# Kernel optimization log

Measured on AMD Instinct MI355X. Metric: run time of the kernel, lower is better.

## Reference

```python
import jax, jax.numpy as jnp
import numpy as np

N = 100000      # nodes
E = 1600000     # edges (before self loops)
F_IN = 128
HID = 32
H = 4
OUT = 32
NEG_SLOPE = 0.2


def setup_inputs() -> dict:
    key = jax.random.key(0)
    ks = jax.random.split(key, 10)
    x = jax.random.normal(ks[0], (N, F_IN), jnp.float32)
    edge_index = jax.random.randint(ks[1], (2, E), 0, N, jnp.int32)
    s1 = 1.0 / np.sqrt(F_IN)
    s2 = 1.0 / np.sqrt(H * HID)
    W1 = jax.random.normal(ks[2], (F_IN, H * HID), jnp.float32) * s1
    a_src1 = jax.random.normal(ks[3], (H, HID), jnp.float32) * 0.1
    a_dst1 = jax.random.normal(ks[4], (H, HID), jnp.float32) * 0.1
    b1 = jnp.zeros((H * HID,), jnp.float32)
    W2 = jax.random.normal(ks[5], (H * HID, OUT), jnp.float32) * s2
    a_src2 = jax.random.normal(ks[6], (1, OUT), jnp.float32) * 0.1
    a_dst2 = jax.random.normal(ks[7], (1, OUT), jnp.float32) * 0.1
    b2 = jnp.zeros((OUT,), jnp.float32)
    return {"x": x, "edge_index": edge_index, "W1": W1, "a_src1": a_src1,
            "a_dst1": a_dst1, "b1": b1, "W2": W2, "a_src2": a_src2,
            "a_dst2": a_dst2, "b2": b2}


def gat_conv(x, src, dst, W, a_src, a_dst, b, heads, out_ch):
    # PyG GATConv (concat=True) with self loops already appended to src/dst.
    n = x.shape[0]
    h = (x @ W).reshape(n, heads, out_ch)                 # [N,H,C]
    alpha_s = jnp.sum(h * a_src, axis=-1)                 # [N,H]
    alpha_d = jnp.sum(h * a_dst, axis=-1)                 # [N,H]
    e = jax.nn.leaky_relu(alpha_s[src] + alpha_d[dst], NEG_SLOPE)  # [E',H]
    # segment softmax over destination nodes (self loops => every segment nonempty)
    emax = jax.ops.segment_max(e, dst, num_segments=n)
    ex = jnp.exp(e - emax[dst])
    denom = jax.ops.segment_sum(ex, dst, num_segments=n)
    alpha = ex / denom[dst]                               # [E',H]
    msg = h[src] * alpha[:, :, None]                      # [E',H,C]
    out = jax.ops.segment_sum(msg, dst, num_segments=n)   # [N,H,C]
    return out.reshape(n, heads * out_ch) + b


def reference(x, edge_index, W1, a_src1, a_dst1, b1, W2, a_src2, a_dst2, b2):
    loops = jnp.arange(N, dtype=edge_index.dtype)
    src = jnp.concatenate([edge_index[0], loops])
    dst = jnp.concatenate([edge_index[1], loops])
    h = gat_conv(x, src, dst, W1, a_src1, a_dst1, b1, H, HID)
    h = jax.nn.relu(h)                                    # dropout: eval mode, no-op
    out = gat_conv(h, src, dst, W2, a_src2, a_dst2, b2, 1, OUT)
    return out
```

## Files before the change

### kernel.cpp

```cpp
#include <hip/hip_runtime.h>
#include <hip/hip_fp16.h>

#define NEG 0.2f
#define EPB 4096
#define BSH 6
#define SLOT 48
#define CAP 1280
#define KBMAX 1664

typedef _Float16 half8 __attribute__((ext_vector_type(8)));
typedef float f32x4 __attribute__((ext_vector_type(4)));

__device__ inline __half2 pun_h2(float f) { union { float f; __half2 h; } u; u.f = f; return u.h; }
__device__ inline float pun_f(__half2 h) { union { float f; __half2 h; } u; u.h = h; return u.f; }

__global__ void k_prep(const float* __restrict__ W1, const float* __restrict__ W2,
                       half8* __restrict__ Wp, half8* __restrict__ W2p,
                       int* __restrict__ gcount, int KB) {
    int b = blockIdx.x;
    if (b < 8) {
        int u = b * 256 + threadIdx.x;
        int s = u >> 9, tn = (u >> 6) & 7, lane = u & 63;
        int quad = lane >> 4, c = lane & 15;
        half8 v;
#pragma unroll
        for (int j = 0; j < 8; ++j)
            v[j] = (_Float16)W1[(s * 32 + quad * 8 + j) * 128 + tn * 16 + c];
        Wp[u] = v;
    } else if (b < 10) {
        int u = (b - 8) * 256 + threadIdx.x;
        int n = u >> 8, s = (u >> 6) & 3, lane = u & 63;
        int quad = lane >> 4, c = lane & 15;
        half8 v;
#pragma unroll
        for (int j = 0; j < 8; ++j)
            v[j] = (_Float16)W2[(s * 32 + quad * 8 + j) * 32 + n * 16 + c];
        W2p[u] = v;
    } else {
        int i = (b - 10) * 256 + threadIdx.x;
        if (i < KB) gcount[i] = 0;
    }
}

__global__ __launch_bounds__(256) void k_pA(const float* __restrict__ x,
                                            const half8* __restrict__ Wp,
                                            const float* __restrict__ a_s,
                                            const float* __restrict__ a_d,
                                            __half* __restrict__ h1h,
                                            float* __restrict__ as1,
                                            float* __restrict__ ad1, int N,
                                            const int* __restrict__ srcp,
                                            const int* __restrict__ dstp,
                                            int* __restrict__ gcount,
                                            int2* __restrict__ ebuf,
                                            int E, int KB, int ngemm) {
    __shared__ _Float16 xa[64][136];
    __shared__ int lh[KBMAX];
    int t = threadIdx.x;

    if (blockIdx.x >= ngemm) {
        int blk = blockIdx.x - ngemm;
        int base0 = blk * EPB;
        int ss[16], dd[16];
#pragma unroll
        for (int j = 0; j < 16; ++j) {
            int i = base0 + j * 256 + t;
            if (i < E) { ss[j] = srcp[i]; dd[j] = dstp[i]; } else dd[j] = -1;
        }
        for (int i = t; i < KB; i += 256) lh[i] = 0;
        __syncthreads();
#pragma unroll
        for (int j = 0; j < 16; ++j)
            if (dd[j] >= 0) atomicAdd(&lh[dd[j] >> BSH], 1);
        __syncthreads();
        for (int b = t; b < KB; b += 256) {
            int c = lh[b];
            if (c > 0) lh[b] = atomicAdd(&gcount[b], c);
        }
        __syncthreads();
#pragma unroll
        for (int j = 0; j < 16; ++j) {
            if (dd[j] >= 0) {
                int b = dd[j] >> BSH;
                int pos = atomicAdd(&lh[b], 1);
                ebuf[(size_t)b * CAP + pos] = int2{ss[j], dd[j]};
            }
        }
        return;
    }

    int row0 = blockIdx.x * 64;
    {
        int row = t >> 2;
        int col0 = (t & 3) * 32;
        int gr = row0 + row;
        const float4* xsrc = (const float4*)&x[(size_t)gr * 128 + col0];
#pragma unroll
        for (int m = 0; m < 4; ++m) {
            float4 p0, p1;
            if (gr < N) { p0 = xsrc[m * 2]; p1 = xsrc[m * 2 + 1]; }
            else { p0 = float4{0,0,0,0}; p1 = float4{0,0,0,0}; }
            _Float16* dstq = &xa[row][col0 + m * 8];
            dstq[0] = (_Float16)p0.x; dstq[1] = (_Float16)p0.y;
            dstq[2] = (_Float16)p0.z; dstq[3] = (_Float16)p0.w;
            dstq[4] = (_Float16)p1.x; dstq[5] = (_Float16)p1.y;
            dstq[6] = (_Float16)p1.z; dstq[7] = (_Float16)p1.w;
        }
    }
    __syncthreads();

    int w = t >> 6;
    int lane = t & 63;
    int quad = lane >> 4, c = lane & 15;

    f32x4 acc[8];
#pragma unroll
    for (int i = 0; i < 8; ++i) acc[i] = f32x4{0, 0, 0, 0};

#pragma unroll
    for (int s = 0; s < 4; ++s) {
        half8 a = *(const half8*)&xa[w * 16 + c][s * 32 + quad * 8];
#pragma unroll
        for (int tn = 0; tn < 8; ++tn) {
            half8 b = Wp[(s * 8 + tn) * 64 + lane];
            acc[tn] = __builtin_amdgcn_mfma_f32_16x16x32_f16(a, b, acc[tn], 0, 0, 0);
        }
    }

    float asv[8], adv[8];
#pragma unroll
    for (int tn = 0; tn < 8; ++tn) { asv[tn] = a_s[tn * 16 + c]; adv[tn] = a_d[tn * 16 + c]; }
#pragma unroll
    for (int r = 0; r < 4; ++r) {
        int gr = row0 + w * 16 + quad * 4 + r;
#pragma unroll
        for (int h = 0; h < 4; ++h) {
            float ps = acc[2*h][r] * asv[2*h] + acc[2*h+1][r] * asv[2*h+1];
            float pd = acc[2*h][r] * adv[2*h] + acc[2*h+1][r] * adv[2*h+1];
            ps += __shfl_xor(ps, 1); ps += __shfl_xor(ps, 2);
            ps += __shfl_xor(ps, 4); ps += __shfl_xor(ps, 8);
            pd += __shfl_xor(pd, 1); pd += __shfl_xor(pd, 2);
            pd += __shfl_xor(pd, 4); pd += __shfl_xor(pd, 8);
            if (c == 0 && gr < N) { as1[gr * 4 + h] = ps; ad1[gr * 4 + h] = pd; }
        }
    }

    __syncthreads();
#pragma unroll
    for (int tn = 0; tn < 8; ++tn)
#pragma unroll
        for (int r = 0; r < 4; ++r)
            xa[w * 16 + quad * 4 + r][tn * 16 + c] = (_Float16)acc[tn][r];
    __syncthreads();
    {
        int row = t >> 2;
        int seg = t & 3;
        int gr = row0 + row;
        if (gr < N) {
            float4* gp = (float4*)&h1h[(size_t)gr * 128 + seg * 32];
#pragma unroll
            for (int i = 0; i < 4; ++i)
                gp[i] = *(float4*)&xa[row][seg * 32 + i * 8];
        }
    }
}

__global__ __launch_bounds__(256) void k_aggC(const int2* __restrict__ ebuf,
                                              const int* __restrict__ gcount,
                                              const __half* __restrict__ h1h,
                                              const float* __restrict__ as1,
                                              const float* __restrict__ ad1,
                                              const float* __restrict__ b1,
                                              const half8* __restrict__ W2p,
                                              const float* __restrict__ asw,
                                              const float* __restrict__ adw,
                                              int* __restrict__ csr,
                                              int* __restrict__ counts,
                                              __half* __restrict__ h2h,
                                              float* __restrict__ as2,
                                              float* __restrict__ ad2, int N) {
    __shared__ int lcnt[64];
    __shared__ int lcsr[64 * SLOT];
    __shared__ _Float16 stg[4][16][136];
    int t = threadIdx.x;
    int b = blockIdx.x, d0 = b << BSH;

    if (t < 64) lcnt[t] = 0;
    __syncthreads();

    int ecnt = gcount[b];
    const int2* eb = &ebuf[(size_t)b * CAP];
    for (int i = t; i < ecnt; i += 256) {
        int2 e = eb[i];
        int li = e.y - d0;
        int r = atomicAdd(&lcnt[li], 1);
        lcsr[li * SLOT + r] = e.x;
    }
    __syncthreads();

    {
        int4* gc = (int4*)&csr[(size_t)d0 * SLOT];
        const int4* lc = (const int4*)lcsr;
#pragma unroll
        for (int u = 0; u < 3; ++u) gc[t + 256 * u] = lc[t + 256 * u];
        if (t < 64 && d0 + t < N) counts[d0 + t] = lcnt[t];
    }

    int w = t >> 6, lane = t & 63;
    int q = lane >> 5, c4 = lane & 31;
    int head4 = c4 >> 3;
    const __half2* hp = (const __half2*)h1h;
    float4 bv4 = *(const float4*)&b1[4 * c4];

    for (int i = 0; i < 8; ++i) {
        int li = w * 16 + 2 * i + q;
        int dst = d0 + li;
        bool valid = dst < N;
        int cnt = valid ? lcnt[li] : 0;
        int cbase = li * SLOT;
        float adv = valid ? ad1[dst * 4 + head4] : 0.f;
        float a0 = 0.f, a1 = 0.f, a2 = 0.f, a3 = 0.f, den = 0.f;
        float g0 = 0.f, g1 = 0.f, g2 = 0.f, g3 = 0.f, dn2 = 0.f;
        if (valid) {
            float es = as1[dst * 4 + head4] + adv;
            es = es > 0.f ? es : NEG * es;
            float xs = __expf(es);
            float2 vv = *(const float2*)&hp[(size_t)dst * 64 + 2 * c4];
            float2 f01 = __half22float2(pun_h2(vv.x));
            float2 f23 = __half22float2(pun_h2(vv.y));
            a0 = xs * f01.x; a1 = xs * f01.y; a2 = xs * f23.x; a3 = xs * f23.y;
            den = xs;
        }
        int e = 0;
        for (; e + 7 < cnt; e += 8) {
            int si[8];
#pragma unroll
            for (int j = 0; j < 8; ++j) si[j] = lcsr[cbase + e + j];
            float ej[8];
#pragma unroll
            for (int j = 0; j < 8; ++j) ej[j] = as1[si[j] * 4 + head4];
            float2 vj[8];
#pragma unroll
            for (int j = 0; j < 8; ++j) vj[j] = *(const float2*)&hp[(size_t)si[j] * 64 + 2 * c4];
#pragma unroll
            for (int j = 0; j < 8; ++j) {
                float ee = ej[j] + adv;
                ee = ee > 0.f ? ee : NEG * ee;
                float xw = __expf(ee);
                float2 f01 = __half22float2(pun_h2(vj[j].x));
                float2 f23 = __half22float2(pun_h2(vj[j].y));
                if ((j & 1) == 0) {
                    a0 += xw * f01.x; a1 += xw * f01.y;
                    a2 += xw * f23.x; a3 += xw * f23.y;
                    den += xw;
                } else {
                    g0 += xw * f01.x; g1 += xw * f01.y;
                    g2 += xw * f23.x; g3 += xw * f23.y;
                    dn2 += xw;
                }
            }
        }
        for (; e + 3 < cnt; e += 4) {
            int si[4];
#pragma unroll
            for (int j = 0; j < 4; ++j) si[j] = lcsr[cbase + e + j];
            float ej[4];
#pragma unroll
            for (int j = 0; j < 4; ++j) ej[j] = as1[si[j] * 4 + head4];
            float2 vj[4];
#pragma unroll
            for (int j = 0; j < 4; ++j) vj[j] = *(const float2*)&hp[(size_t)si[j] * 64 + 2 * c4];
#pragma unroll
            for (int j = 0; j < 4; ++j) {
                float ee = ej[j] + adv;
                ee = ee > 0.f ? ee : NEG * ee;
                float xw = __expf(ee);
                float2 f01 = __half22float2(pun_h2(vj[j].x));
                float2 f23 = __half22float2(pun_h2(vj[j].y));
                if ((j & 1) == 0) {
                    a0 += xw * f01.x; a1 += xw * f01.y;
                    a2 += xw * f23.x; a3 += xw * f23.y;
                    den += xw;
                } else {
                    g0 += xw * f01.x; g1 += xw * f01.y;
                    g2 += xw * f23.x; g3 += xw * f23.y;
                    dn2 += xw;
                }
            }
        }
        for (; e < cnt; ++e) {
            int s0 = lcsr[cbase + e];
            float e0v = as1[s0 * 4 + head4] + adv;
            float2 vv = *(const float2*)&hp[(size_t)s0 * 64 + 2 * c4];
            e0v = e0v > 0.f ? e0v : NEG * e0v;  float x0 = __expf(e0v);
            float2 f01 = __half22float2(pun_h2(vv.x));
            float2 f23 = __half22float2(pun_h2(vv.y));
            g0 += x0 * f01.x; g1 += x0 * f01.y;
            g2 += x0 * f23.x; g3 += x0 * f23.y;
            dn2 += x0;
        }
        a0 += g0; a1 += g1; a2 += g2; a3 += g3; den += dn2;
        float inv = valid ? 1.f / den : 0.f;
        float o0 = a0 * inv + bv4.x;
        float o1 = a1 * inv + bv4.y;
        float o2 = a2 * inv + bv4.z;
        float o3 = a3 * inv + bv4.w;
        o0 = o0 > 0.f ? o0 : 0.f;
        o1 = o1 > 0.f ? o1 : 0.f;
        o2 = o2 > 0.f ? o2 : 0.f;
        o3 = o3 > 0.f ? o3 : 0.f;
        float2 st;
        st.x = pun_f(__floats2half2_rn(o0, o1));
        st.y = pun_f(__floats2half2_rn(o2, o3));
        *(float2*)&stg[w][2 * i + q][4 * c4] = st;
    }

    int quad = lane >> 4, c16 = lane & 15;
    half8 bf[2][4];
#pragma unroll
    for (int n = 0; n < 2; ++n)
#pragma unroll
        for (int s = 0; s < 4; ++s) bf[n][s] = W2p[(n * 4 + s) * 64 + lane];
    float asw0 = asw[c16], asw1 = asw[16 + c16];
    float adw0 = adw[c16], adw1 = adw[16 + c16];

    f32x4 am0 = {0, 0, 0, 0}, am1 = {0, 0, 0, 0};
#pragma unroll
    for (int s = 0; s < 4; ++s) {
        half8 a = *(const half8*)&stg[w][c16][s * 32 + quad * 8];
        am0 = __builtin_amdgcn_mfma_f32_16x16x32_f16(a, bf[0][s], am0, 0, 0, 0);
        am1 = __builtin_amdgcn_mfma_f32_16x16x32_f16(a, bf[1][s], am1, 0, 0, 0);
    }
#pragma unroll
    for (int r = 0; r < 4; ++r) {
        int dst = d0 + w * 16 + quad * 4 + r;
        float ps = am0[r] * asw0 + am1[r] * asw1;
        float pd = am0[r] * adw0 + am1[r] * adw1;
        ps += __shfl_xor(ps, 1); ps += __shfl_xor(ps, 2);
        ps += __shfl_xor(ps, 4); ps += __shfl_xor(ps, 8);
        pd += __shfl_xor(pd, 1); pd += __shfl_xor(pd, 2);
        pd += __shfl_xor(pd, 4); pd += __shfl_xor(pd, 8);
        if (dst < N) {
            h2h[(size_t)dst * 32 + c16]      = __float2half_rn(am0[r]);
            h2h[(size_t)dst * 32 + 16 + c16] = __float2half_rn(am1[r]);
            if (c16 == 0) { as2[dst] = ps; ad2[dst] = pd; }
        }
    }
}

__global__ __launch_bounds__(256) void k_agg2(const __half* __restrict__ h2h,
                                              const float* __restrict__ as2,
                                              const float* __restrict__ ad2,
                                              const int* __restrict__ csr,
                                              const int* __restrict__ counts,
                                              const float* __restrict__ b2,
                                              float* __restrict__ out, int N) {
    int w = threadIdx.x >> 6;
    int lane = threadIdx.x & 63;
    int dst = blockIdx.x * 4 + w;
    if (dst >= N) return;
    int q = lane >> 5;
    int c = lane & 31;
    float adv = ad2[dst];
    int beg = dst * SLOT;
    int cnt = counts[dst];
    float acc = 0.f, den = 0.f;
    if (q == 0) {
        float es = as2[dst] + adv;
        es = es > 0.f ? es : NEG * es;
        float xs = __expf(es);
        acc = xs * __half2float(h2h[(size_t)dst * 32 + c]);
        den = xs;
    }
    int e = q;
    for (; e + 14 < cnt; e += 16) {
        int si[8];
#pragma unroll
        for (int j = 0; j < 8; ++j) si[j] = csr[beg + e + 2 * j];
        float ej[8];
#pragma unroll
        for (int j = 0; j < 8; ++j) ej[j] = as2[si[j]];
        float vj[8];
#pragma unroll
        for (int j = 0; j < 8; ++j) vj[j] = __half2float(h2h[(size_t)si[j] * 32 + c]);
#pragma unroll
        for (int j = 0; j < 8; ++j) {
            float ee = ej[j] + adv;
            ee = ee > 0.f ? ee : NEG * ee;
            float xw = __expf(ee);
            acc += xw * vj[j];
            den += xw;
        }
    }
    for (; e + 6 < cnt; e += 8) {
        int si[4];
#pragma unroll
        for (int j = 0; j < 4; ++j) si[j] = csr[beg + e + 2 * j];
        float ej[4];
#pragma unroll
        for (int j = 0; j < 4; ++j) ej[j] = as2[si[j]];
        float vj[4];
#pragma unroll
        for (int j = 0; j < 4; ++j) vj[j] = __half2float(h2h[(size_t)si[j] * 32 + c]);
#pragma unroll
        for (int j = 0; j < 4; ++j) {
            float ee = ej[j] + adv;
            ee = ee > 0.f ? ee : NEG * ee;
            float xw = __expf(ee);
            acc += xw * vj[j];
            den += xw;
        }
    }
    for (; e < cnt; e += 2) {
        int s0 = csr[beg + e];
        float e0 = as2[s0] + adv;
        float v0 = __half2float(h2h[(size_t)s0 * 32 + c]);
        e0 = e0 > 0.f ? e0 : NEG * e0;  float x0 = __expf(e0);
        acc += x0 * v0;
        den += x0;
    }
    acc += __shfl_xor(acc, 32, 64);
    den += __shfl_xor(den, 32, 64);
    if (q == 0) out[(size_t)dst * 32 + c] = acc / den + b2[c];
}

extern "C" void kernel_launch(void* const* d_in, const int* in_sizes, int n_in,
                              void* d_out, int out_size, void* d_ws, size_t ws_size,
                              hipStream_t stream) {
    const float* x     = (const float*)d_in[0];
    const int*   ei    = (const int*)d_in[1];
    const float* W1    = (const float*)d_in[2];
    const float* as_w1 = (const float*)d_in[3];
    const float* ad_w1 = (const float*)d_in[4];
    const float* b1    = (const float*)d_in[5];
    const float* W2    = (const float*)d_in[6];
    const float* as_w2 = (const float*)d_in[7];
    const float* ad_w2 = (const float*)d_in[8];
    const float* b2    = (const float*)d_in[9];
    float* out = (float*)d_out;

    int N  = in_sizes[0] / 128;
    int E  = in_sizes[1] / 2;
    const int* srcp = ei;
    const int* dstp = ei + E;

    int KB     = (N + 63) >> BSH;
    int ND     = KB << BSH;
    int nblkB  = (E + EPB - 1) / EPB;
    int ngemm  = (N + 63) / 64;

    char* p = (char*)d_ws;
    auto alloc = [&](size_t bytes) -> char* {
        char* r = p;
        p += (bytes + 255) & ~(size_t)255;
        return r;
    };
    __half* h1h    = (__half*)alloc((size_t)N * 128 * 2);
    float*  as1    = (float*)alloc((size_t)N * 4 * 4);
    float*  ad1    = (float*)alloc((size_t)N * 4 * 4);
    __half* h2h    = (__half*)alloc((size_t)N * 32 * 2);
    float*  as2    = (float*)alloc((size_t)N * 4);
    float*  ad2    = (float*)alloc((size_t)N * 4);
    int*    counts = (int*)alloc((size_t)ND * 4);
    int*    csr    = (int*)alloc((size_t)ND * SLOT * 4);
    half8*  Wp     = (half8*)alloc(2048 * 16);
    half8*  W2p    = (half8*)alloc(512 * 16);
    int*    gcount = (int*)alloc((size_t)KB * 4);
    int2*   ebuf   = (int2*)alloc((size_t)KB * CAP * 8);

    k_prep<<<10 + (KB + 255) / 256, 256, 0, stream>>>(W1, W2, Wp, W2p, gcount, KB);
    k_pA<<<ngemm + nblkB, 256, 0, stream>>>(x, Wp, as_w1, ad_w1, h1h, as1, ad1, N,
                                            srcp, dstp, gcount, ebuf, E, KB, ngemm);
    k_aggC<<<KB, 256, 0, stream>>>(ebuf, gcount, h1h, as1, ad1, b1,
                                   W2p, as_w2, ad_w2, csr, counts, h2h, as2, ad2, N);
    k_agg2<<<(N + 3) / 4, 256, 0, stream>>>(h2h, as2, ad2, csr, counts, b2, out, N);
}
```

Measured before the change: 285.6 us.

## Pack edges into 32-bit words and rebuild local CSR in layer-2 aggregation

Edges in the bucket buffer are packed as one 32-bit word, with the source in the low 20 bits and the local destination in the upper bits, which halves the buffer traffic. The layer-1 aggregation no longer writes a global CSR and counts array. The layer-2 aggregation re-reads the packed bucket and rebuilds the per-block CSR in shared memory, processing 64 destinations per block with split accumulators. The x staging store is also vectorised to a half8 write. The packing assumes node ids fit in 20 bits, and the bucket is now read twice instead of the CSR once.

```diff
diff --git a/kernel.cpp b/kernel.cpp
--- a/kernel.cpp
+++ b/kernel.cpp
@@ -7,6 +7,8 @@
 #define SLOT 48
 #define CAP 1280
 #define KBMAX 1664
+#define SRCBITS 20
+#define SRCMASK 0xFFFFFu
 
 typedef _Float16 half8 __attribute__((ext_vector_type(8)));
 typedef float f32x4 __attribute__((ext_vector_type(4)));
@@ -52,7 +54,7 @@
                                             const int* __restrict__ srcp,
                                             const int* __restrict__ dstp,
                                             int* __restrict__ gcount,
-                                            int2* __restrict__ ebuf,
+                                            unsigned* __restrict__ ebuf,
                                             int E, int KB, int ngemm) {
     __shared__ _Float16 xa[64][136];
     __shared__ int lh[KBMAX];
@@ -83,7 +85,8 @@
             if (dd[j] >= 0) {
                 int b = dd[j] >> BSH;
                 int pos = atomicAdd(&lh[b], 1);
-                ebuf[(size_t)b * CAP + pos] = int2{ss[j], dd[j]};
+                ebuf[(size_t)b * CAP + pos] =
+                    (unsigned)ss[j] | ((unsigned)(dd[j] & 63) << SRCBITS);
             }
         }
         return;
@@ -100,11 +103,12 @@
             float4 p0, p1;
             if (gr < N) { p0 = xsrc[m * 2]; p1 = xsrc[m * 2 + 1]; }
             else { p0 = float4{0,0,0,0}; p1 = float4{0,0,0,0}; }
-            _Float16* dstq = &xa[row][col0 + m * 8];
-            dstq[0] = (_Float16)p0.x; dstq[1] = (_Float16)p0.y;
-            dstq[2] = (_Float16)p0.z; dstq[3] = (_Float16)p0.w;
-            dstq[4] = (_Float16)p1.x; dstq[5] = (_Float16)p1.y;
-            dstq[6] = (_Float16)p1.z; dstq[7] = (_Float16)p1.w;
+            half8 v;
+            v[0] = (_Float16)p0.x; v[1] = (_Float16)p0.y;
+            v[2] = (_Float16)p0.z; v[3] = (_Float16)p0.w;
+            v[4] = (_Float16)p1.x; v[5] = (_Float16)p1.y;
+            v[6] = (_Float16)p1.z; v[7] = (_Float16)p1.w;
+            *(half8*)&xa[row][col0 + m * 8] = v;
         }
     }
     __syncthreads();
@@ -165,7 +169,7 @@
     }
 }
 
-__global__ __launch_bounds__(256) void k_aggC(const int2* __restrict__ ebuf,
+__global__ __launch_bounds__(256) void k_aggC(const unsigned* __restrict__ ebuf,
                                               const int* __restrict__ gcount,
                                               const __half* __restrict__ h1h,
                                               const float* __restrict__ as1,
@@ -174,8 +178,6 @@
                                               const half8* __restrict__ W2p,
                                               const float* __restrict__ asw,
                                               const float* __restrict__ adw,
-                                              int* __restrict__ csr,
-                                              int* __restrict__ counts,
                                               __half* __restrict__ h2h,
                                               float* __restrict__ as2,
                                               float* __restrict__ ad2, int N) {
@@ -189,22 +191,14 @@
     __syncthreads();
 
     int ecnt = gcount[b];
-    const int2* eb = &ebuf[(size_t)b * CAP];
+    const unsigned* eb = &ebuf[(size_t)b * CAP];
     for (int i = t; i < ecnt; i += 256) {
-        int2 e = eb[i];
-        int li = e.y - d0;
+        unsigned e = eb[i];
+        int li = e >> SRCBITS;
         int r = atomicAdd(&lcnt[li], 1);
-        lcsr[li * SLOT + r] = e.x;
-    }
-    __syncthreads();
-
-    {
-        int4* gc = (int4*)&csr[(size_t)d0 * SLOT];
-        const int4* lc = (const int4*)lcsr;
-#pragma unroll
-        for (int u = 0; u < 3; ++u) gc[t + 256 * u] = lc[t + 256 * u];
-        if (t < 64 && d0 + t < N) counts[d0 + t] = lcnt[t];
-    }
+        lcsr[li * SLOT + r] = (int)(e & SRCMASK);
+    }
+    __syncthreads();
 
     int w = t >> 6, lane = t & 63;
     int q = lane >> 5, c4 = lane & 31;
@@ -348,80 +342,99 @@
     }
 }
 
-__global__ __launch_bounds__(256) void k_agg2(const __half* __restrict__ h2h,
+__global__ __launch_bounds__(256) void k_agg2(const unsigned* __restrict__ ebuf,
+                                              const int* __restrict__ gcount,
+                                              const __half* __restrict__ h2h,
                                               const float* __restrict__ as2,
                                               const float* __restrict__ ad2,
-                                              const int* __restrict__ csr,
-                                              const int* __restrict__ counts,
                                               const float* __restrict__ b2,
                                               float* __restrict__ out, int N) {
-    int w = threadIdx.x >> 6;
-    int lane = threadIdx.x & 63;
-    int dst = blockIdx.x * 4 + w;
-    if (dst >= N) return;
-    int q = lane >> 5;
-    int c = lane & 31;
-    float adv = ad2[dst];
-    int beg = dst * SLOT;
-    int cnt = counts[dst];
-    float acc = 0.f, den = 0.f;
-    if (q == 0) {
-        float es = as2[dst] + adv;
-        es = es > 0.f ? es : NEG * es;
-        float xs = __expf(es);
-        acc = xs * __half2float(h2h[(size_t)dst * 32 + c]);
-        den = xs;
-    }
-    int e = q;
-    for (; e + 14 < cnt; e += 16) {
-        int si[8];
-#pragma unroll
-        for (int j = 0; j < 8; ++j) si[j] = csr[beg + e + 2 * j];
-        float ej[8];
-#pragma unroll
-        for (int j = 0; j < 8; ++j) ej[j] = as2[si[j]];
-        float vj[8];
-#pragma unroll
-        for (int j = 0; j < 8; ++j) vj[j] = __half2float(h2h[(size_t)si[j] * 32 + c]);
-#pragma unroll
-        for (int j = 0; j < 8; ++j) {
-            float ee = ej[j] + adv;
-            ee = ee > 0.f ? ee : NEG * ee;
-            float xw = __expf(ee);
-            acc += xw * vj[j];
-            den += xw;
-        }
-    }
-    for (; e + 6 < cnt; e += 8) {
-        int si[4];
-#pragma unroll
-        for (int j = 0; j < 4; ++j) si[j] = csr[beg + e + 2 * j];
-        float ej[4];
-#pragma unroll
-        for (int j = 0; j < 4; ++j) ej[j] = as2[si[j]];
-        float vj[4];
-#pragma unroll
-        for (int j = 0; j < 4; ++j) vj[j] = __half2float(h2h[(size_t)si[j] * 32 + c]);
-#pragma unroll
-        for (int j = 0; j < 4; ++j) {
-            float ee = ej[j] + adv;
-            ee = ee > 0.f ? ee : NEG * ee;
-            float xw = __expf(ee);
-            acc += xw * vj[j];
-            den += xw;
-        }
-    }
-    for (; e < cnt; e += 2) {
-        int s0 = csr[beg + e];
-        float e0 = as2[s0] + adv;
-        float v0 = __half2float(h2h[(size_t)s0 * 32 + c]);
-        e0 = e0 > 0.f ? e0 : NEG * e0;  float x0 = __expf(e0);
-        acc += x0 * v0;
-        den += x0;
-    }
-    acc += __shfl_xor(acc, 32, 64);
-    den += __shfl_xor(den, 32, 64);
-    if (q == 0) out[(size_t)dst * 32 + c] = acc / den + b2[c];
+    __shared__ int lcnt[64];
+    __shared__ int lcsr[64 * SLOT];
+    int t = threadIdx.x;
+    int b = blockIdx.x, d0 = b << BSH;
+
+    if (t < 64) lcnt[t] = 0;
+    __syncthreads();
+
+    int ecnt = gcount[b];
+    const unsigned* eb = &ebuf[(size_t)b * CAP];
+    for (int i = t; i < ecnt; i += 256) {
+        unsigned e = eb[i];
+        int li = e >> SRCBITS;
+        int r = atomicAdd(&lcnt[li], 1);
+        lcsr[li * SLOT + r] = (int)(e & SRCMASK);
+    }
+    __syncthreads();
+
+    int w = t >> 6, lane = t & 63;
+    int q = lane >> 5, c = lane & 31;
+
+    for (int i = 0; i < 8; ++i) {
+        int li = w * 16 + 2 * i + q;
+        int dst = d0 + li;
+        bool valid = dst < N;
+        int cnt = valid ? lcnt[li] : 0;
+        int cbase = li * SLOT;
+        float adv = valid ? ad2[dst] : 0.f;
+        float accA = 0.f, denA = 0.f, accB = 0.f, denB = 0.f;
+        if (valid) {
+            float es = as2[dst] + adv;
+            es = es > 0.f ? es : NEG * es;
+            float xs = __expf(es);
+            accA = xs * __half2float(h2h[(size_t)dst * 32 + c]);
+            denA = xs;
+        }
+        int e = 0;
+        for (; e + 7 < cnt; e += 8) {
+            int si[8];
+#pragma unroll
+            for (int j = 0; j < 8; ++j) si[j] = lcsr[cbase + e + j];
+            float ej[8];
+#pragma unroll
+            for (int j = 0; j < 8; ++j) ej[j] = as2[si[j]];
+            float vj[8];
+#pragma unroll
+            for (int j = 0; j < 8; ++j) vj[j] = __half2float(h2h[(size_t)si[j] * 32 + c]);
+#pragma unroll
+            for (int j = 0; j < 8; ++j) {
+                float ee = ej[j] + adv;
+                ee = ee > 0.f ? ee : NEG * ee;
+                float xw = __expf(ee);
+                if ((j & 1) == 0) { accA += xw * vj[j]; denA += xw; }
+                else              { accB += xw * vj[j]; denB += xw; }
+            }
+        }
+        for (; e + 3 < cnt; e += 4) {
+            int si[4];
+#pragma unroll
+            for (int j = 0; j < 4; ++j) si[j] = lcsr[cbase + e + j];
+            float ej[4];
+#pragma unroll
+            for (int j = 0; j < 4; ++j) ej[j] = as2[si[j]];
+            float vj[4];
+#pragma unroll
+            for (int j = 0; j < 4; ++j) vj[j] = __half2float(h2h[(size_t)si[j] * 32 + c]);
+#pragma unroll
+            for (int j = 0; j < 4; ++j) {
+                float ee = ej[j] + adv;
+                ee = ee > 0.f ? ee : NEG * ee;
+                float xw = __expf(ee);
+                if ((j & 1) == 0) { accA += xw * vj[j]; denA += xw; }
+                else              { accB += xw * vj[j]; denB += xw; }
+            }
+        }
+        for (; e < cnt; ++e) {
+            int s0 = lcsr[cbase + e];
+            float e0 = as2[s0] + adv;
+            float v0 = __half2float(h2h[(size_t)s0 * 32 + c]);
+            e0 = e0 > 0.f ? e0 : NEG * e0;  float x0 = __expf(e0);
+            accB += x0 * v0;
+            denB += x0;
+        }
+        if (valid)
+            out[(size_t)dst * 32 + c] = (accA + accB) / (denA + denB) + b2[c];
+    }
 }
 
 extern "C" void kernel_launch(void* const* d_in, const int* in_sizes, int n_in,
@@ -445,7 +458,6 @@
     const int* dstp = ei + E;
 
     int KB     = (N + 63) >> BSH;
-    int ND     = KB << BSH;
     int nblkB  = (E + EPB - 1) / EPB;
     int ngemm  = (N + 63) / 64;
 
@@ -455,23 +467,21 @@
         p += (bytes + 255) & ~(size_t)255;
         return r;
     };
-    __half* h1h    = (__half*)alloc((size_t)N * 128 * 2);
-    float*  as1    = (float*)alloc((size_t)N * 4 * 4);
-    float*  ad1    = (float*)alloc((size_t)N * 4 * 4);
-    __half* h2h    = (__half*)alloc((size_t)N * 32 * 2);
-    float*  as2    = (float*)alloc((size_t)N * 4);
-    float*  ad2    = (float*)alloc((size_t)N * 4);
-    int*    counts = (int*)alloc((size_t)ND * 4);
-    int*    csr    = (int*)alloc((size_t)ND * SLOT * 4);
-    half8*  Wp     = (half8*)alloc(2048 * 16);
-    half8*  W2p    = (half8*)alloc(512 * 16);
-    int*    gcount = (int*)alloc((size_t)KB * 4);
-    int2*   ebuf   = (int2*)alloc((size_t)KB * CAP * 8);
+    __half*   h1h    = (__half*)alloc((size_t)N * 128 * 2);
+    float*    as1    = (float*)alloc((size_t)N * 4 * 4);
+    float*    ad1    = (float*)alloc((size_t)N * 4 * 4);
+    __half*   h2h    = (__half*)alloc((size_t)N * 32 * 2);
+    float*    as2    = (float*)alloc((size_t)N * 4);
+    float*    ad2    = (float*)alloc((size_t)N * 4);
+    half8*    Wp     = (half8*)alloc(2048 * 16);
+    half8*    W2p    = (half8*)alloc(512 * 16);
+    int*      gcount = (int*)alloc((size_t)KB * 4);
+    unsigned* ebuf   = (unsigned*)alloc((size_t)KB * CAP * 4);
 
     k_prep<<<10 + (KB + 255) / 256, 256, 0, stream>>>(W1, W2, Wp, W2p, gcount, KB);
     k_pA<<<ngemm + nblkB, 256, 0, stream>>>(x, Wp, as_w1, ad_w1, h1h, as1, ad1, N,
                                             srcp, dstp, gcount, ebuf, E, KB, ngemm);
     k_aggC<<<KB, 256, 0, stream>>>(ebuf, gcount, h1h, as1, ad1, b1,
-                                   W2p, as_w2, ad_w2, csr, counts, h2h, as2, ad2, N);
-    k_agg2<<<(N + 3) / 4, 256, 0, stream>>>(h2h, as2, ad2, csr, counts, b2, out, N);
+                                   W2p, as_w2, ad_w2, h2h, as2, ad2, N);
+    k_agg2<<<KB, 256, 0, stream>>>(ebuf, gcount, h2h, as2, ad2, b2, out, N);
 }
```

After: 272.1 us. -4.7%, faster.
